# Performance work log

Hardware: AMD Instinct MI355X
Metric: run time of the kernel (lower is better)

## Reference

```python
import jax, jax.numpy as jnp
import numpy as np

N = 50000
E = 800000
F_IN = 500
H = 5          # heads
C = 32         # per-head channels
HID = H * C    # 160
NC = 20        # num_classes
G = 8          # number of graphs in batch
SLOPE_ATT = 0.2   # GATConv attention leaky slope (PyG default)
SLOPE_ACT = 0.01  # F.leaky_relu default


def _layernorm(x, scale, bias, eps=1e-5):
    mu = jnp.mean(x, axis=-1, keepdims=True)
    var = jnp.var(x, axis=-1, keepdims=True)
    return (x - mu) * jax.lax.rsqrt(var + eps) * scale + bias


def _edge_softmax(logits, dst, num_nodes):
    # segment softmax over incoming edges of each destination node
    m = jax.ops.segment_max(logits, dst, num_segments=num_nodes)
    ex = jnp.exp(logits - m[dst])
    s = jax.ops.segment_sum(ex, dst, num_segments=num_nodes)
    return ex / (s[dst] + 1e-16)


def _gat_layer(x, src, dst, W, a_src, a_dst, b):
    n = x.shape[0]
    h = (x @ W).reshape(n, H, C)                       # [N,H,C]
    al_s = jnp.einsum('nhc,hc->nh', h, a_src)          # [N,H]
    al_d = jnp.einsum('nhc,hc->nh', h, a_dst)
    logits = jax.nn.leaky_relu(al_s[src] + al_d[dst], SLOPE_ATT)  # [Et,H]
    alpha = _edge_softmax(logits, dst, n)              # [Et,H]
    msg = h[src] * alpha[..., None]                    # [Et,H,C]
    out = jax.ops.segment_sum(msg, dst, num_segments=n).reshape(n, HID) + b
    return out, alpha


def setup_inputs():
    key = jax.random.key(0)
    ks = jax.random.split(key, 24)
    p = lambda k, shp: jax.random.normal(k, shp, jnp.float32) * 0.05
    x = jax.random.normal(ks[0], (N, F_IN), jnp.float32)
    edge_index = jax.random.randint(ks[1], (2, E), 0, N, jnp.int64)
    batch = jnp.sort(jax.random.randint(ks[2], (N,), 0, G, jnp.int64))
    return {
        'x': x, 'edge_index': edge_index, 'batch': batch,
        'W1': p(ks[3], (F_IN, HID)), 'a_src1': p(ks[4], (H, C)), 'a_dst1': p(ks[5], (H, C)), 'b1': jnp.zeros((HID,), jnp.float32),
        'ln1_s': jnp.ones((HID,), jnp.float32), 'ln1_b': jnp.zeros((HID,), jnp.float32),
        'W2': p(ks[6], (HID, HID)), 'a_src2': p(ks[7], (H, C)), 'a_dst2': p(ks[8], (H, C)), 'b2': jnp.zeros((HID,), jnp.float32),
        'ln2_s': jnp.ones((HID,), jnp.float32), 'ln2_b': jnp.zeros((HID,), jnp.float32),
        'Wm': p(ks[9], (HID, HID)), 'bm': jnp.zeros((HID,), jnp.float32),
        'Wmlp1': p(ks[10], (HID, HID)), 'bmlp1': jnp.zeros((HID,), jnp.float32),
        'ln3_s': jnp.ones((HID,), jnp.float32), 'ln3_b': jnp.zeros((HID,), jnp.float32),
        'Wmlp2': p(ks[11], (HID, NC)), 'bmlp2': jnp.zeros((NC,), jnp.float32),
    }


def reference(x, edge_index, batch, W1, a_src1, a_dst1, b1, ln1_s, ln1_b,
              W2, a_src2, a_dst2, b2, ln2_s, ln2_b, Wm, bm,
              Wmlp1, bmlp1, ln3_s, ln3_b, Wmlp2, bmlp2):
    n = x.shape[0]
    # PyG GATConv adds self-loops by default
    loops = jnp.arange(n, dtype=edge_index.dtype)
    src = jnp.concatenate([edge_index[0], loops])
    dst = jnp.concatenate([edge_index[1], loops])

    h1, alpha1 = _gat_layer(x, src, dst, W1, a_src1, a_dst1, b1)
    h1 = jax.nn.leaky_relu(h1, SLOPE_ACT)
    h1 = _layernorm(h1, ln1_s, ln1_b)      # dropout = identity at eval

    h2, alpha2 = _gat_layer(h1, src, dst, W2, a_src2, a_dst2, b2)
    h2 = jax.nn.leaky_relu(h2, SLOPE_ACT)
    h2 = _layernorm(h2, ln2_s, ln2_b)

    xo = jax.nn.leaky_relu(h2 @ Wm + bm, SLOPE_ACT)   # [N,HID]

    # global_mean_pool over batch assignment
    sums = jax.ops.segment_sum(xo, batch, num_segments=G)
    cnts = jax.ops.segment_sum(jnp.ones((n, 1), xo.dtype), batch, num_segments=G)
    pooled = sums / jnp.maximum(cnts, 1.0)            # [G,HID]

    z = pooled @ Wmlp1 + bmlp1
    z = jax.nn.relu(_layernorm(z, ln3_s, ln3_b))
    rec = z @ Wmlp2 + bmlp2                           # [G,NC]
    return xo, rec, alpha1, alpha2
```

## Files before the change

### kernel.cpp

```cpp
#include <hip/hip_runtime.h>
#include <hip/hip_bf16.h>
#include <cstdint>
#include <cstddef>

#define NN   50000
#define EE   800000
#define ET_  (EE + NN)
#define FIN  500
#define HID_ 160
#define NC_  20
#define GG   8
#define GB1  ((NN + 63) / 64)
#define NK1  16
#define NK2  5

typedef __attribute__((ext_vector_type(8))) short ab8;
typedef __attribute__((ext_vector_type(4))) float f4;

static __device__ __forceinline__ unsigned short f2bf(float v) {
    union { float f; uint32_t u; } c; c.f = v;
    uint32_t r = c.u + 0x7FFFu + ((c.u >> 16) & 1u);
    return (unsigned short)(r >> 16);
}

static __device__ __forceinline__ float2 bf2f2(uint32_t u) {
    union { uint32_t u; float f; } a, b;
    a.u = u << 16;
    b.u = u & 0xffff0000u;
    return make_float2(a.f, b.f);
}

static __device__ __forceinline__ int lbound_i(const int* arr, int n, int val) {
    int lo = 0, hi = n;
    while (lo < hi) { int mid = (lo + hi) >> 1; if (arr[mid] < val) lo = mid + 1; else hi = mid; }
    return lo;
}

__global__ __launch_bounds__(256) void k_hist(const int* __restrict__ ei, int* __restrict__ deg) {
    int e = blockIdx.x * 256 + threadIdx.x;
    if (e >= ET_) return;
    int d = (e < EE) ? ei[EE + e] : (e - EE);
    atomicAdd(&deg[d], 1);
}

__global__ __launch_bounds__(256) void k_scan1(const int* __restrict__ deg, int* __restrict__ rowptr,
                                               int* __restrict__ bsum) {
    __shared__ int s[256];
    int t = threadIdx.x;
    int base = blockIdx.x * 1024 + t * 4;
    int v0 = (base + 0 < NN) ? deg[base + 0] : 0;
    int v1 = (base + 1 < NN) ? deg[base + 1] : 0;
    int v2 = (base + 2 < NN) ? deg[base + 2] : 0;
    int v3 = (base + 3 < NN) ? deg[base + 3] : 0;
    int tot = v0 + v1 + v2 + v3;
    s[t] = tot;
    __syncthreads();
    for (int off = 1; off < 256; off <<= 1) {
        int y = (t >= off) ? s[t - off] : 0;
        __syncthreads();
        s[t] += y;
        __syncthreads();
    }
    int excl = s[t] - tot;
    if (t == 255) bsum[blockIdx.x] = s[255];
    if (base + 0 < NN) rowptr[base + 0] = excl;  excl += v0;
    if (base + 1 < NN) rowptr[base + 1] = excl;  excl += v1;
    if (base + 2 < NN) rowptr[base + 2] = excl;  excl += v2;
    if (base + 3 < NN) rowptr[base + 3] = excl;
}

__global__ void k_scan2(int* __restrict__ bsum, int nb) {
    int t = threadIdx.x;
    int v = (t < nb) ? bsum[t] : 0;
    int orig = v;
    for (int off = 1; off < 64; off <<= 1) {
        int y = __shfl_up(v, off);
        if (t >= off) v += y;
    }
    if (t < nb) bsum[t] = v - orig;
}

__global__ __launch_bounds__(256) void k_scan3(int* __restrict__ rowptr, const int* __restrict__ bsum,
                                               int* __restrict__ cursor) {
    int i = blockIdx.x * 256 + threadIdx.x;
    if (i < NN) {
        int r = rowptr[i] + bsum[i >> 10];
        rowptr[i] = r;
        cursor[i] = r;
    }
    if (i == NN) rowptr[NN] = ET_;
}

__global__ __launch_bounds__(256) void k_scatter(const int* __restrict__ ei, int* __restrict__ cursor,
                                                 int* __restrict__ esrc) {
    int e = blockIdx.x * 256 + threadIdx.x;
    if (e >= ET_) return;
    int s, d;
    if (e < EE) { s = ei[e]; d = ei[EE + e]; } else { s = e - EE; d = e - EE; }
    int slot = atomicAdd(&cursor[d], 1);
    esrc[slot] = s;
}

__global__ __launch_bounds__(256) void k_prep_all(const float* __restrict__ W1, ab8* __restrict__ B1,
                                                  const float* __restrict__ W2, ab8* __restrict__ B2,
                                                  const float* __restrict__ Wm, ab8* __restrict__ Bm,
                                                  float* __restrict__ pooled) {
    int idx = blockIdx.x * 256 + threadIdx.x;
    if (idx < GG * HID_) pooled[idx] = 0.f;
    const int C1 = NK1 * 10 * 64;
    const int C2 = NK2 * 10 * 64;
    const float* W; ab8* Bo; int K, cidx;
    if (idx < C1)                { W = W1; Bo = B1; K = FIN;  cidx = idx; }
    else if (idx < C1 + C2)      { W = W2; Bo = B2; K = HID_; cidx = idx - C1; }
    else if (idx < C1 + 2 * C2)  { W = Wm; Bo = Bm; K = HID_; cidx = idx - C1 - C2; }
    else return;
    int s = cidx / 640, r = cidx % 640;
    int t = r >> 6, l = r & 63;
    int fr = l & 15, q = l >> 4;
    int n  = t * 16 + fr;
    int k0 = s * 32 + q * 8;
    unsigned short pk[8];
#pragma unroll
    for (int j = 0; j < 8; j++) {
        int k = k0 + j;
        pk[j] = (k < K) ? f2bf(W[(size_t)k * HID_ + n]) : (unsigned short)0;
    }
    Bo[cidx] = *reinterpret_cast<ab8*>(pk);
}

__global__ __launch_bounds__(256) void k_conv_x(const float* __restrict__ x, ab8* __restrict__ Apk) {
    int idx = blockIdx.x * 256 + threadIdx.x;
    int tid = idx & 255;
    int s   = (idx >> 8) & (NK1 - 1);
    int blk = idx >> 12;
    int l = tid & 63, w = tid >> 6;
    int fr = l & 15, q = l >> 4;
    int row = blk * 64 + w * 16 + fr;
    int k0 = s * 32 + q * 8;
    unsigned short pk[8] = {0, 0, 0, 0, 0, 0, 0, 0};
    if (row < NN) {
        const float* xr = &x[(size_t)row * FIN];
        if (k0 + 8 <= FIN) {
            const float4* s4 = reinterpret_cast<const float4*>(&xr[k0]);
            float4 u = s4[0], v = s4[1];
            pk[0] = f2bf(u.x); pk[1] = f2bf(u.y); pk[2] = f2bf(u.z); pk[3] = f2bf(u.w);
            pk[4] = f2bf(v.x); pk[5] = f2bf(v.y); pk[6] = f2bf(v.z); pk[7] = f2bf(v.w);
        } else {
#pragma unroll
            for (int j = 0; j < 8; j++)
                if (k0 + j < FIN) pk[j] = f2bf(xr[k0 + j]);
        }
    }
    Apk[idx] = *reinterpret_cast<ab8*>(pk);
}

static __device__ __forceinline__ void gemm_body(const ab8* __restrict__ Apk,
                                                 const ab8* __restrict__ Bpk, int nk,
                                                 float* __restrict__ C, __hip_bfloat16* __restrict__ Cb,
                                                 int M,
                                                 const float* __restrict__ bias, int act,
                                                 const float* __restrict__ asrc, const float* __restrict__ adst,
                                                 float* __restrict__ als_o, float* __restrict__ ald_o,
                                                 const int* __restrict__ batch_p, float* __restrict__ pooled) {
    int tid  = threadIdx.x;
    int lane = tid & 63;
    int w    = tid >> 6;
    int fr   = lane & 15;
    int q    = lane >> 4;
    int row0 = blockIdx.x * 64;

    f4 acc[10];
#pragma unroll
    for (int t = 0; t < 10; t++) acc[t] = (f4)0.f;

    const ab8* bb  = Bpk + lane;
    const ab8* apk = Apk + (size_t)blockIdx.x * nk * 256 + tid;

    ab8 bcur[10], bnx[10];
#pragma unroll
    for (int t = 0; t < 10; t++) bcur[t] = bb[t * 64];
    ab8 a0 = apk[0];
    ab8 a1 = apk[256];
    for (int s = 0; s < nk; s++) {
        if (s + 1 < nk) {
#pragma unroll
            for (int t = 0; t < 10; t++) bnx[t] = bb[((s + 1) * 10 + t) * 64];
        }
        ab8 a2 = (ab8)0;
        if (s + 2 < nk) a2 = apk[(s + 2) * 256];
#pragma unroll
        for (int t = 0; t < 10; t++)
            acc[t] = __builtin_amdgcn_mfma_f32_16x16x32_bf16(a0, bcur[t], acc[t], 0, 0, 0);
        a0 = a1; a1 = a2;
#pragma unroll
        for (int t = 0; t < 10; t++) bcur[t] = bnx[t];
    }

    if (als_o) {
        float av_s[10], av_d[10];
#pragma unroll
        for (int t = 0; t < 10; t++) { av_s[t] = asrc[t * 16 + fr]; av_d[t] = adst[t * 16 + fr]; }
#pragma unroll
        for (int i = 0; i < 4; i++) {
            int r = row0 + w * 16 + q * 4 + i;
            float ps[5], pd[5];
#pragma unroll
            for (int h = 0; h < 5; h++) {
                ps[h] = acc[2 * h][i] * av_s[2 * h] + acc[2 * h + 1][i] * av_s[2 * h + 1];
                pd[h] = acc[2 * h][i] * av_d[2 * h] + acc[2 * h + 1][i] * av_d[2 * h + 1];
            }
#pragma unroll
            for (int off = 8; off >= 1; off >>= 1)
#pragma unroll
                for (int h = 0; h < 5; h++) {
                    ps[h] += __shfl_xor(ps[h], off);
                    pd[h] += __shfl_xor(pd[h], off);
                }
            if (fr == 0 && r < M) {
#pragma unroll
                for (int h = 0; h < 5; h++) {
                    als_o[(size_t)r * 8 + h] = ps[h];
                    ald_o[(size_t)r * 8 + h] = pd[h];
                }
            }
        }
    }

    int gu = -2;
    if (pooled) {
        int rhi = row0 + 63; if (rhi >= M) rhi = M - 1;
        int gl = batch_p[row0], gh = batch_p[rhi];
        gu = (gl == gh) ? gl : -1;
    }
    float psum[10];
#pragma unroll
    for (int t = 0; t < 10; t++) psum[t] = 0.f;

    int rbase = row0 + w * 16 + q * 4;
#pragma unroll
    for (int t = 0; t < 10; t++) {
        int col = t * 16 + fr;
        float bv = bias ? bias[col] : 0.f;
#pragma unroll
        for (int i = 0; i < 4; i++) {
            int r = rbase + i;
            float v = acc[t][i] + bv;
            if (act) v = v > 0.f ? v : 0.01f * v;
            if (r < M) {
                if (C)  C[(size_t)r * HID_ + col] = v;
                if (Cb) *reinterpret_cast<unsigned short*>(&Cb[(size_t)r * HID_ + col]) = f2bf(v);
                if (gu >= 0) psum[t] += v;
                else if (gu == -1) atomicAdd(&pooled[batch_p[r] * HID_ + col], v);
            }
        }
    }
    if (gu >= 0) {
#pragma unroll
        for (int t = 0; t < 10; t++) {
            psum[t] += __shfl_xor(psum[t], 16);
            psum[t] += __shfl_xor(psum[t], 32);
        }
        if (q == 0) {
#pragma unroll
            for (int t = 0; t < 10; t++)
                atomicAdd(&pooled[gu * HID_ + t * 16 + fr], psum[t]);
        }
    }
}

__global__ __launch_bounds__(256) void k_gemm_pk(const ab8* __restrict__ Apk,
                                                 const ab8* __restrict__ Bpk, int nk,
                                                 float* __restrict__ C, __hip_bfloat16* __restrict__ Cb,
                                                 int M,
                                                 const float* __restrict__ bias, int act,
                                                 const float* __restrict__ asrc, const float* __restrict__ adst,
                                                 float* __restrict__ als_o, float* __restrict__ ald_o,
                                                 const int* __restrict__ batch_p, float* __restrict__ pooled) {
    gemm_body(Apk, Bpk, nk, C, Cb, M, bias, act, asrc, adst, als_o, ald_o, batch_p, pooled);
}

__global__ __launch_bounds__(256) void k_att_agg(const int* __restrict__ rowptr,
                                                 const int* __restrict__ esrc,
                                                 const float* __restrict__ als, const float* __restrict__ ald,
                                                 const __hip_bfloat16* __restrict__ hmat,
                                                 float* __restrict__ alphap,
                                                 float* __restrict__ invb,
                                                 const float* __restrict__ bias,
                                                 const float* __restrict__ lns, const float* __restrict__ lnb,
                                                 uint4* __restrict__ xpk) {
    __shared__ float sExp[4][64 * 5];
    __shared__ int   sSrc[4][64];
    int wv   = threadIdx.x >> 6;
    int lane = threadIdx.x & 63;
    int node = blockIdx.x * 4 + wv;
    if (node >= NN) return;
    int start = rowptr[node], end = rowptr[node + 1];
    int deg = end - start;
    bool fits = (deg <= 64);
    float4 dd4 = *reinterpret_cast<const float4*>(&ald[(size_t)node * 8]);
    float  dd5 = ald[(size_t)node * 8 + 4];
    float ad[5] = {dd4.x, dd4.y, dd4.z, dd4.w, dd5};

    float sm[5] = {0.f, 0.f, 0.f, 0.f, 0.f};
    for (int j = start + lane; j < end; j += 64) {
        int sy = esrc[j];
        int idx = j - start;
        if (fits) sSrc[wv][idx] = sy;
        const float* as = &als[(size_t)sy * 8];
        float4 a4 = *reinterpret_cast<const float4*>(as);
        float  a5 = as[4];
        float asv[5] = {a4.x, a4.y, a4.z, a4.w, a5};
#pragma unroll
        for (int h = 0; h < 5; h++) {
            float l = asv[h] + ad[h];
            l = l > 0.f ? l : 0.2f * l;
            float ex = __expf(fminf(l, 60.f));
            sm[h] += ex;
            if (fits) sExp[wv][idx * 5 + h] = ex;
            else      alphap[(size_t)j * 5 + h] = ex;
        }
    }
#pragma unroll
    for (int off = 32; off >= 1; off >>= 1)
#pragma unroll
        for (int h = 0; h < 5; h++) sm[h] += __shfl_xor(sm[h], off);
    float inv[5];
#pragma unroll
    for (int h = 0; h < 5; h++) inv[h] = 1.f / (sm[h] + 1e-16f);
    if (lane == 0) {
        float* ip = &invb[(size_t)node * 8];
        ip[0] = inv[0]; ip[1] = inv[1]; ip[2] = inv[2]; ip[3] = inv[3]; ip[4] = inv[4];
    }
    if (fits && lane < deg) {
#pragma unroll
        for (int h = 0; h < 5; h++) sExp[wv][lane * 5 + h] *= inv[h];
    }

    int h0 = lane >> 4;
    bool lo16 = lane < 16;
    int c01 = 2 * lane;
    int c2  = 128 + 2 * lane;
    float2 A0 = make_float2(0.f, 0.f), A1 = make_float2(0.f, 0.f);
    float2 A2 = make_float2(0.f, 0.f), A3 = make_float2(0.f, 0.f);
    float2 H0 = make_float2(0.f, 0.f), H1 = make_float2(0.f, 0.f);
    float2 H2 = make_float2(0.f, 0.f), H3 = make_float2(0.f, 0.f);

    if (fits) {
        int idx = 0;
        for (; idx + 3 < deg; idx += 4) {
            int s0 = sSrc[wv][idx], s1 = sSrc[wv][idx + 1];
            int s2 = sSrc[wv][idx + 2], s3 = sSrc[wv][idx + 3];
            float w0 = sExp[wv][(idx + 0) * 5 + h0];
            float w1 = sExp[wv][(idx + 1) * 5 + h0];
            float w2 = sExp[wv][(idx + 2) * 5 + h0];
            float w3 = sExp[wv][(idx + 3) * 5 + h0];
            const unsigned short* r0 = (const unsigned short*)&hmat[(size_t)s0 * HID_];
            const unsigned short* r1 = (const unsigned short*)&hmat[(size_t)s1 * HID_];
            const unsigned short* r2 = (const unsigned short*)&hmat[(size_t)s2 * HID_];
            const unsigned short* r3 = (const unsigned short*)&hmat[(size_t)s3 * HID_];
            float2 f0 = bf2f2(*reinterpret_cast<const uint32_t*>(&r0[c01]));
            float2 f1 = bf2f2(*reinterpret_cast<const uint32_t*>(&r1[c01]));
            float2 f2 = bf2f2(*reinterpret_cast<const uint32_t*>(&r2[c01]));
            float2 f3 = bf2f2(*reinterpret_cast<const uint32_t*>(&r3[c01]));
            A0.x += w0 * f0.x; A0.y += w0 * f0.y;
            A1.x += w1 * f1.x; A1.y += w1 * f1.y;
            A2.x += w2 * f2.x; A2.y += w2 * f2.y;
            A3.x += w3 * f3.x; A3.y += w3 * f3.y;
            if (lo16) {
                float u0 = sExp[wv][(idx + 0) * 5 + 4];
                float u1 = sExp[wv][(idx + 1) * 5 + 4];
                float u2 = sExp[wv][(idx + 2) * 5 + 4];
                float u3 = sExp[wv][(idx + 3) * 5 + 4];
                float2 g0 = bf2f2(*reinterpret_cast<const uint32_t*>(&r0[c2]));
                float2 g1 = bf2f2(*reinterpret_cast<const uint32_t*>(&r1[c2]));
                float2 g2 = bf2f2(*reinterpret_cast<const uint32_t*>(&r2[c2]));
                float2 g3 = bf2f2(*reinterpret_cast<const uint32_t*>(&r3[c2]));
                H0.x += u0 * g0.x; H0.y += u0 * g0.y;
                H1.x += u1 * g1.x; H1.y += u1 * g1.y;
                H2.x += u2 * g2.x; H2.y += u2 * g2.y;
                H3.x += u3 * g3.x; H3.y += u3 * g3.y;
            }
        }
        for (; idx < deg; idx++) {
            int s0 = sSrc[wv][idx];
            float w0 = sExp[wv][idx * 5 + h0];
            const unsigned short* r0 = (const unsigned short*)&hmat[(size_t)s0 * HID_];
            float2 f0 = bf2f2(*reinterpret_cast<const uint32_t*>(&r0[c01]));
            A0.x += w0 * f0.x; A0.y += w0 * f0.y;
            if (lo16) {
                float u0 = sExp[wv][idx * 5 + 4];
                float2 g0 = bf2f2(*reinterpret_cast<const uint32_t*>(&r0[c2]));
                H0.x += u0 * g0.x; H0.y += u0 * g0.y;
            }
        }
    } else {
        for (int j = start; j < end; j++) {
            int s0 = esrc[j];
            float w0 = alphap[(size_t)j * 5 + h0] * inv[h0];
            const unsigned short* r0 = (const unsigned short*)&hmat[(size_t)s0 * HID_];
            float2 f0 = bf2f2(*reinterpret_cast<const uint32_t*>(&r0[c01]));
            A0.x += w0 * f0.x; A0.y += w0 * f0.y;
            if (lo16) {
                float u0 = alphap[(size_t)j * 5 + 4] * inv[4];
                float2 g0 = bf2f2(*reinterpret_cast<const uint32_t*>(&r0[c2]));
                H0.x += u0 * g0.x; H0.y += u0 * g0.y;
            }
        }
    }
    float2 A = make_float2(A0.x + A1.x + A2.x + A3.x, A0.y + A1.y + A2.y + A3.y);
    float2 Hh = make_float2(H0.x + H1.x + H2.x + H3.x, H0.y + H1.y + H2.y + H3.y);

    float2 bb = *reinterpret_cast<const float2*>(&bias[c01]);
    float v0 = A.x + bb.x;  v0 = v0 > 0.f ? v0 : 0.01f * v0;
    float v1 = A.y + bb.y;  v1 = v1 > 0.f ? v1 : 0.01f * v1;
    float v2 = 0.f, v3 = 0.f;
    if (lo16) {
        float2 b2 = *reinterpret_cast<const float2*>(&bias[c2]);
        v2 = Hh.x + b2.x; v2 = v2 > 0.f ? v2 : 0.01f * v2;
        v3 = Hh.y + b2.y; v3 = v3 > 0.f ? v3 : 0.01f * v3;
    }
    float s  = v0 + v1 + v2 + v3;
    float sq = v0 * v0 + v1 * v1 + v2 * v2 + v3 * v3;
#pragma unroll
    for (int off = 32; off >= 1; off >>= 1) {
        s  += __shfl_xor(s, off);
        sq += __shfl_xor(sq, off);
    }
    float m = s * (1.f / 160.f);
    float r = rsqrtf(sq * (1.f / 160.f) - m * m + 1e-5f);
    uint32_t pk1, pk2 = 0u;
    {
        float2 sc = *reinterpret_cast<const float2*>(&lns[c01]);
        float2 bi = *reinterpret_cast<const float2*>(&lnb[c01]);
        pk1 = (uint32_t)f2bf((v0 - m) * r * sc.x + bi.x)
            | ((uint32_t)f2bf((v1 - m) * r * sc.y + bi.y) << 16);
    }
    if (lo16) {
        float2 sc = *reinterpret_cast<const float2*>(&lns[c2]);
        float2 bi = *reinterpret_cast<const float2*>(&lnb[c2]);
        pk2 = (uint32_t)f2bf((v2 - m) * r * sc.x + bi.x)
            | ((uint32_t)f2bf((v3 - m) * r * sc.y + bi.y) << 16);
    }
    int j = lane;
    int srcb = (j < 16) ? (4 * j) : (4 * ((j - 16) & 15));
    uint32_t a0w = __shfl(pk1, srcb + 0), a1w = __shfl(pk1, srcb + 1);
    uint32_t a2w = __shfl(pk1, srcb + 2), a3w = __shfl(pk1, srcb + 3);
    uint32_t b0w = __shfl(pk2, srcb + 0), b1w = __shfl(pk2, srcb + 1);
    uint32_t b2w = __shfl(pk2, srcb + 2), b3w = __shfl(pk2, srcb + 3);
    if (j < 20) {
        uint4 val;
        val.x = (j < 16) ? a0w : b0w;
        val.y = (j < 16) ? a1w : b1w;
        val.z = (j < 16) ? a2w : b2w;
        val.w = (j < 16) ? a3w : b3w;
        int blk = node >> 6, wq = (node >> 4) & 3, fr = node & 15;
        int ks = j >> 2, q = j & 3;
        size_t cidx = (size_t)(blk * NK2 + ks) * 256 + wq * 64 + q * 16 + fr;
        xpk[cidx] = val;
    }
}

__global__ __launch_bounds__(256) void k_alpha(const int* __restrict__ ei,
                                               const float* __restrict__ als, const float* __restrict__ ald,
                                               const float* __restrict__ invb,
                                               float* __restrict__ alpha_out) {
    int e = blockIdx.x * 256 + threadIdx.x;
    if (e >= ET_) return;
    int s, d;
    if (e < EE) { s = ei[e]; d = ei[EE + e]; } else { s = e - EE; d = e - EE; }
    const float* as = &als[(size_t)s * 8];
    float4 a4 = *reinterpret_cast<const float4*>(as);
    float  a5 = as[4];
    float asv[5] = {a4.x, a4.y, a4.z, a4.w, a5};
    const float* adp = &ald[(size_t)d * 8];
    float4 d4 = *reinterpret_cast<const float4*>(adp);
    float  d5 = adp[4];
    float adv[5] = {d4.x, d4.y, d4.z, d4.w, d5};
    const float* ip = &invb[(size_t)d * 8];
    float4 i4 = *reinterpret_cast<const float4*>(ip);
    float  i5 = ip[4];
    float ivv[5] = {i4.x, i4.y, i4.z, i4.w, i5};
    float* ao = &alpha_out[(size_t)e * 5];
#pragma unroll
    for (int h = 0; h < 5; h++) {
        float l = asv[h] + adv[h];
        l = l > 0.f ? l : 0.2f * l;
        float ex = __expf(fminf(l, 60.f));
        ao[h] = ex * ivv[h];
    }
}

__global__ __launch_bounds__(256) void k_mlp(const float* __restrict__ pooled, const int* __restrict__ batch,
                                             const float* __restrict__ W1, const float* __restrict__ b1,
                                             const float* __restrict__ lns, const float* __restrict__ lnb,
                                             const float* __restrict__ W2, const float* __restrict__ b2,
                                             float* __restrict__ rec) {
    __shared__ float P[GG][HID_];
    __shared__ float Z[GG][HID_];
    __shared__ float mu[GG], rr[GG], ic[GG];
    int t = threadIdx.x;
    if (t < GG) {
        int lo = lbound_i(batch, NN, t), hi = lbound_i(batch, NN, t + 1);
        ic[t] = 1.f / fmaxf((float)(hi - lo), 1.f);
    }
    __syncthreads();
    for (int i = t; i < GG * HID_; i += 256) P[i / HID_][i % HID_] = pooled[i] * ic[i / HID_];
    __syncthreads();
    for (int i = t; i < GG * HID_; i += 256) {
        int g = i / HID_, j = i % HID_;
        float acc = b1[j];
        for (int k = 0; k < HID_; k++) acc += P[g][k] * W1[k * HID_ + j];
        Z[g][j] = acc;
    }
    __syncthreads();
    if (t < GG) {
        float s = 0.f, sq = 0.f;
        for (int k = 0; k < HID_; k++) { float z = Z[t][k]; s += z; sq += z * z; }
        float m = s / (float)HID_;
        mu[t] = m;
        rr[t] = rsqrtf(sq / (float)HID_ - m * m + 1e-5f);
    }
    __syncthreads();
    for (int i = t; i < GG * HID_; i += 256) {
        int g = i / HID_, j = i % HID_;
        float z = (Z[g][j] - mu[g]) * rr[g] * lns[j] + lnb[j];
        Z[g][j] = fmaxf(z, 0.f);
    }
    __syncthreads();
    for (int i = t; i < GG * NC_; i += 256) {
        int g = i / NC_, j = i % NC_;
        float acc = b2[j];
        for (int k = 0; k < HID_; k++) acc += Z[g][k] * W2[k * NC_ + j];
        rec[g * NC_ + j] = acc;
    }
}

extern "C" void kernel_launch(void* const* d_in, const int* in_sizes, int n_in,
                              void* d_out, int out_size, void* d_ws, size_t ws_size,
                              hipStream_t stream) {
    const float* x    = (const float*)d_in[0];
    const int*   ei   = (const int*)d_in[1];
    const int*   batch= (const int*)d_in[2];
    const float* W1   = (const float*)d_in[3];
    const float* as1  = (const float*)d_in[4];
    const float* ad1  = (const float*)d_in[5];
    const float* b1   = (const float*)d_in[6];
    const float* ln1s = (const float*)d_in[7];
    const float* ln1b = (const float*)d_in[8];
    const float* W2   = (const float*)d_in[9];
    const float* as2  = (const float*)d_in[10];
    const float* ad2  = (const float*)d_in[11];
    const float* b2   = (const float*)d_in[12];
    const float* ln2s = (const float*)d_in[13];
    const float* ln2b = (const float*)d_in[14];
    const float* Wm   = (const float*)d_in[15];
    const float* bm   = (const float*)d_in[16];
    const float* Wm1  = (const float*)d_in[17];
    const float* bm1  = (const float*)d_in[18];
    const float* ln3s = (const float*)d_in[19];
    const float* ln3b = (const float*)d_in[20];
    const float* Wm2  = (const float*)d_in[21];
    const float* bm2  = (const float*)d_in[22];

    float* out    = (float*)d_out;
    float* xo     = out;
    float* rec    = out + (size_t)NN * HID_;
    float* alpha1 = rec + GG * NC_;
    float* alpha2 = alpha1 + (size_t)ET_ * 5;

    char* w = (char*)d_ws;
    auto carve = [&](size_t bytes) { char* p = w; w += (bytes + 255) & ~(size_t)255; return p; };
    int*   deg    = (int*)carve((size_t)NN * 4);
    int*   rowptr = (int*)carve((size_t)(NN + 1) * 4);
    int*   cursor = (int*)carve((size_t)NN * 4);
    int*   esrc   = (int*)carve((size_t)ET_ * 4);
    int*   bsum   = (int*)carve(64 * 4);
    __hip_bfloat16* hbuf = (__hip_bfloat16*)carve((size_t)NN * HID_ * 2);
    uint4* xpk    = (uint4*)carve((size_t)GB1 * NK2 * 256 * 16);
    float* alphap = (float*)carve((size_t)ET_ * 5 * 4);
    float* als    = (float*)carve((size_t)NN * 8 * 4);
    float* ald    = (float*)carve((size_t)NN * 8 * 4);
    float* invb   = (float*)carve((size_t)NN * 8 * 4);
    float* pooled = (float*)carve((size_t)GG * HID_ * 4);
    ab8*   B1pk   = (ab8*)carve((size_t)NK1 * 10 * 64 * 16);
    ab8*   B2pk   = (ab8*)carve((size_t)NK2 * 10 * 64 * 16);
    ab8*   Bmpk   = (ab8*)carve((size_t)NK2 * 10 * 64 * 16);
    ab8*   Apk    = (ab8*)d_out;

    hipMemsetAsync(deg, 0, (size_t)NN * 4, stream);
    k_hist<<<(ET_ + 255) / 256, 256, 0, stream>>>(ei, deg);
    int nb = (NN + 1023) / 1024;
    k_scan1<<<nb, 256, 0, stream>>>(deg, rowptr, bsum);
    k_scan2<<<1, 64, 0, stream>>>(bsum, nb);
    k_scan3<<<(NN + 1 + 255) / 256, 256, 0, stream>>>(rowptr, bsum, cursor);
    k_scatter<<<(ET_ + 255) / 256, 256, 0, stream>>>(ei, cursor, esrc);

    const int PREP = NK1 * 10 * 64 + 2 * NK2 * 10 * 64;
    k_prep_all<<<(PREP + 255) / 256, 256, 0, stream>>>(W1, B1pk, W2, B2pk, Wm, Bmpk, pooled);
    k_conv_x<<<GB1 * NK1, 256, 0, stream>>>(x, Apk);

    const int NWB = (NN + 3) / 4;
    const int EB  = (ET_ + 255) / 256;

    k_gemm_pk<<<GB1, 256, 0, stream>>>(Apk, B1pk, NK1, nullptr, hbuf, NN, nullptr, 0,
                                       as1, ad1, als, ald, nullptr, nullptr);
    k_att_agg<<<NWB, 256, 0, stream>>>(rowptr, esrc, als, ald, hbuf, alphap, invb,
                                       b1, ln1s, ln1b, xpk);
    k_alpha<<<EB, 256, 0, stream>>>(ei, als, ald, invb, alpha1);

    k_gemm_pk<<<GB1, 256, 0, stream>>>((const ab8*)xpk, B2pk, NK2, nullptr, hbuf, NN, nullptr, 0,
                                       as2, ad2, als, ald, nullptr, nullptr);
    k_att_agg<<<NWB, 256, 0, stream>>>(rowptr, esrc, als, ald, hbuf, alphap, invb,
                                       b2, ln2s, ln2b, xpk);
    k_alpha<<<EB, 256, 0, stream>>>(ei, als, ald, invb, alpha2);

    k_gemm_pk<<<GB1, 256, 0, stream>>>((const ab8*)xpk, Bmpk, NK2, xo, nullptr, NN, bm, 1,
                                       nullptr, nullptr, nullptr, nullptr, batch, pooled);
    k_mlp<<<1, 256, 0, stream>>>(pooled, batch, Wm1, bm1, ln3s, ln3b, Wm2, bm2, rec);
}
```

Measured before the change: 643.2 us.

## Horizontally fuse independent kernels to cut launches and overlap small stages

Result: faster. 612.2 us (-4.8%).

```diff
diff --git a/kernel.cpp b/kernel.cpp
--- a/kernel.cpp
+++ b/kernel.cpp
@@ -13,6 +13,7 @@
 #define GB1  ((NN + 63) / 64)
 #define NK1  16
 #define NK2  5
+#define EBH  ((ET_ + 255) / 256)
 
 typedef __attribute__((ext_vector_type(8))) short ab8;
 typedef __attribute__((ext_vector_type(4))) float f4;
@@ -36,11 +37,66 @@
     return lo;
 }
 
-__global__ __launch_bounds__(256) void k_hist(const int* __restrict__ ei, int* __restrict__ deg) {
-    int e = blockIdx.x * 256 + threadIdx.x;
-    if (e >= ET_) return;
-    int d = (e < EE) ? ei[EE + e] : (e - EE);
-    atomicAdd(&deg[d], 1);
+__global__ __launch_bounds__(256) void k_prep0(const float* __restrict__ W1, ab8* __restrict__ B1,
+                                               const float* __restrict__ W2, ab8* __restrict__ B2,
+                                               const float* __restrict__ Wm, ab8* __restrict__ Bm,
+                                               float* __restrict__ pooled, int* __restrict__ deg) {
+    int idx = blockIdx.x * 256 + threadIdx.x;
+    if (idx < NN) deg[idx] = 0;
+    if (idx < GG * HID_) pooled[idx] = 0.f;
+    const int C1 = NK1 * 10 * 64;
+    const int C2 = NK2 * 10 * 64;
+    const float* W; ab8* Bo; int K, cidx;
+    if (idx < C1)                { W = W1; Bo = B1; K = FIN;  cidx = idx; }
+    else if (idx < C1 + C2)      { W = W2; Bo = B2; K = HID_; cidx = idx - C1; }
+    else if (idx < C1 + 2 * C2)  { W = Wm; Bo = Bm; K = HID_; cidx = idx - C1 - C2; }
+    else return;
+    int s = cidx / 640, r = cidx % 640;
+    int t = r >> 6, l = r & 63;
+    int fr = l & 15, q = l >> 4;
+    int n  = t * 16 + fr;
+    int k0 = s * 32 + q * 8;
+    unsigned short pk[8];
+#pragma unroll
+    for (int j = 0; j < 8; j++) {
+        int k = k0 + j;
+        pk[j] = (k < K) ? f2bf(W[(size_t)k * HID_ + n]) : (unsigned short)0;
+    }
+    Bo[cidx] = *reinterpret_cast<ab8*>(pk);
+}
+
+__global__ __launch_bounds__(256) void k_hist_conv(const int* __restrict__ ei, int* __restrict__ deg,
+                                                   const float* __restrict__ x, ab8* __restrict__ Apk) {
+    if (blockIdx.x < EBH) {
+        int e = blockIdx.x * 256 + threadIdx.x;
+        if (e >= ET_) return;
+        int d = (e < EE) ? ei[EE + e] : (e - EE);
+        atomicAdd(&deg[d], 1);
+        return;
+    }
+    int idx = (blockIdx.x - EBH) * 256 + threadIdx.x;
+    int tid = idx & 255;
+    int s   = (idx >> 8) & (NK1 - 1);
+    int blk = idx >> 12;
+    int l = tid & 63, w = tid >> 6;
+    int fr = l & 15, q = l >> 4;
+    int row = blk * 64 + w * 16 + fr;
+    int k0 = s * 32 + q * 8;
+    unsigned short pk[8] = {0, 0, 0, 0, 0, 0, 0, 0};
+    if (row < NN) {
+        const float* xr = &x[(size_t)row * FIN];
+        if (k0 + 8 <= FIN) {
+            const float4* s4 = reinterpret_cast<const float4*>(&xr[k0]);
+            float4 u = s4[0], v = s4[1];
+            pk[0] = f2bf(u.x); pk[1] = f2bf(u.y); pk[2] = f2bf(u.z); pk[3] = f2bf(u.w);
+            pk[4] = f2bf(v.x); pk[5] = f2bf(v.y); pk[6] = f2bf(v.z); pk[7] = f2bf(v.w);
+        } else {
+#pragma unroll
+            for (int j = 0; j < 8; j++)
+                if (k0 + j < FIN) pk[j] = f2bf(xr[k0 + j]);
+        }
+    }
+    Apk[idx] = *reinterpret_cast<ab8*>(pk);
 }
 
 __global__ __launch_bounds__(256) void k_scan1(const int* __restrict__ deg, int* __restrict__ rowptr,
@@ -101,60 +157,8 @@
     esrc[slot] = s;
 }
 
-__global__ __launch_bounds__(256) void k_prep_all(const float* __restrict__ W1, ab8* __restrict__ B1,
-                                                  const float* __restrict__ W2, ab8* __restrict__ B2,
-                                                  const float* __restrict__ Wm, ab8* __restrict__ Bm,
-                                                  float* __restrict__ pooled) {
-    int idx = blockIdx.x * 256 + threadIdx.x;
-    if (idx < GG * HID_) pooled[idx] = 0.f;
-    const int C1 = NK1 * 10 * 64;
-    const int C2 = NK2 * 10 * 64;
-    const float* W; ab8* Bo; int K, cidx;
-    if (idx < C1)                { W = W1; Bo = B1; K = FIN;  cidx = idx; }
-    else if (idx < C1 + C2)      { W = W2; Bo = B2; K = HID_; cidx = idx - C1; }
-    else if (idx < C1 + 2 * C2)  { W = Wm; Bo = Bm; K = HID_; cidx = idx - C1 - C2; }
-    else return;
-    int s = cidx / 640, r = cidx % 640;
-    int t = r >> 6, l = r & 63;
-    int fr = l & 15, q = l >> 4;
-    int n  = t * 16 + fr;
-    int k0 = s * 32 + q * 8;
-    unsigned short pk[8];
-#pragma unroll
-    for (int j = 0; j < 8; j++) {
-        int k = k0 + j;
-        pk[j] = (k < K) ? f2bf(W[(size_t)k * HID_ + n]) : (unsigned short)0;
-    }
-    Bo[cidx] = *reinterpret_cast<ab8*>(pk);
-}
-
-__global__ __launch_bounds__(256) void k_conv_x(const float* __restrict__ x, ab8* __restrict__ Apk) {
-    int idx = blockIdx.x * 256 + threadIdx.x;
-    int tid = idx & 255;
-    int s   = (idx >> 8) & (NK1 - 1);
-    int blk = idx >> 12;
-    int l = tid & 63, w = tid >> 6;
-    int fr = l & 15, q = l >> 4;
-    int row = blk * 64 + w * 16 + fr;
-    int k0 = s * 32 + q * 8;
-    unsigned short pk[8] = {0, 0, 0, 0, 0, 0, 0, 0};
-    if (row < NN) {
-        const float* xr = &x[(size_t)row * FIN];
-        if (k0 + 8 <= FIN) {
-            const float4* s4 = reinterpret_cast<const float4*>(&xr[k0]);
-            float4 u = s4[0], v = s4[1];
-            pk[0] = f2bf(u.x); pk[1] = f2bf(u.y); pk[2] = f2bf(u.z); pk[3] = f2bf(u.w);
-            pk[4] = f2bf(v.x); pk[5] = f2bf(v.y); pk[6] = f2bf(v.z); pk[7] = f2bf(v.w);
-        } else {
-#pragma unroll
-            for (int j = 0; j < 8; j++)
-                if (k0 + j < FIN) pk[j] = f2bf(xr[k0 + j]);
-        }
-    }
-    Apk[idx] = *reinterpret_cast<ab8*>(pk);
-}
-
-static __device__ __forceinline__ void gemm_body(const ab8* __restrict__ Apk,
+static __device__ __forceinline__ void gemm_body(int blk,
+                                                 const ab8* __restrict__ Apk,
                                                  const ab8* __restrict__ Bpk, int nk,
                                                  float* __restrict__ C, __hip_bfloat16* __restrict__ Cb,
                                                  int M,
@@ -167,14 +171,14 @@
     int w    = tid >> 6;
     int fr   = lane & 15;
     int q    = lane >> 4;
-    int row0 = blockIdx.x * 64;
+    int row0 = blk * 64;
 
     f4 acc[10];
 #pragma unroll
     for (int t = 0; t < 10; t++) acc[t] = (f4)0.f;
 
     const ab8* bb  = Bpk + lane;
-    const ab8* apk = Apk + (size_t)blockIdx.x * nk * 256 + tid;
+    const ab8* apk = Apk + (size_t)blk * nk * 256 + tid;
 
     ab8 bcur[10], bnx[10];
 #pragma unroll
@@ -276,7 +280,55 @@
                                                  const float* __restrict__ asrc, const float* __restrict__ adst,
                                                  float* __restrict__ als_o, float* __restrict__ ald_o,
                                                  const int* __restrict__ batch_p, float* __restrict__ pooled) {
-    gemm_body(Apk, Bpk, nk, C, Cb, M, bias, act, asrc, adst, als_o, ald_o, batch_p, pooled);
+    gemm_body(blockIdx.x, Apk, Bpk, nk, C, Cb, M, bias, act, asrc, adst, als_o, ald_o, batch_p, pooled);
+}
+
+static __device__ __forceinline__ void alpha_body(int e, const int* __restrict__ ei,
+                                                  const float* __restrict__ als, const float* __restrict__ ald,
+                                                  const float* __restrict__ invb,
+                                                  float* __restrict__ alpha_out) {
+    if (e >= ET_) return;
+    int s, d;
+    if (e < EE) { s = ei[e]; d = ei[EE + e]; } else { s = e - EE; d = e - EE; }
+    const float* as = &als[(size_t)s * 8];
+    float4 a4 = *reinterpret_cast<const float4*>(as);
+    float  a5 = as[4];
+    float asv[5] = {a4.x, a4.y, a4.z, a4.w, a5};
+    const float* adp = &ald[(size_t)d * 8];
+    float4 d4 = *reinterpret_cast<const float4*>(adp);
+    float  d5 = adp[4];
+    float adv[5] = {d4.x, d4.y, d4.z, d4.w, d5};
+    const float* ip = &invb[(size_t)d * 8];
+    float4 i4 = *reinterpret_cast<const float4*>(ip);
+    float  i5 = ip[4];
+    float ivv[5] = {i4.x, i4.y, i4.z, i4.w, i5};
+    float* ao = &alpha_out[(size_t)e * 5];
+#pragma unroll
+    for (int h = 0; h < 5; h++) {
+        float l = asv[h] + adv[h];
+        l = l > 0.f ? l : 0.2f * l;
+        float ex = __expf(fminf(l, 60.f));
+        ao[h] = ex * ivv[h];
+    }
+}
+
+__global__ __launch_bounds__(256) void k_gemm_alpha(const ab8* __restrict__ Apk,
+                                                    const ab8* __restrict__ Bpk, int nk,
+                                                    float* __restrict__ C, __hip_bfloat16* __restrict__ Cb,
+                                                    int M,
+                                                    const float* __restrict__ bias, int act,
+                                                    const float* __restrict__ asrc, const float* __restrict__ adst,
+                                                    float* __restrict__ als_o, float* __restrict__ ald_o,
+                                                    const int* __restrict__ batch_p, float* __restrict__ pooled,
+                                                    const int* __restrict__ ei,
+                                                    const float* __restrict__ als_r, const float* __restrict__ ald_r,
+                                                    const float* __restrict__ invb, float* __restrict__ alpha_out) {
+    if (blockIdx.x < GB1) {
+        gemm_body(blockIdx.x, Apk, Bpk, nk, C, Cb, M, bias, act, asrc, adst, als_o, ald_o, batch_p, pooled);
+    } else {
+        int e = (blockIdx.x - GB1) * 256 + threadIdx.x;
+        alpha_body(e, ei, als_r, ald_r, invb, alpha_out);
+    }
 }
 
 __global__ __launch_bounds__(256) void k_att_agg(const int* __restrict__ rowptr,
@@ -460,36 +512,6 @@
     }
 }
 
-__global__ __launch_bounds__(256) void k_alpha(const int* __restrict__ ei,
-                                               const float* __restrict__ als, const float* __restrict__ ald,
-                                               const float* __restrict__ invb,
-                                               float* __restrict__ alpha_out) {
-    int e = blockIdx.x * 256 + threadIdx.x;
-    if (e >= ET_) return;
-    int s, d;
-    if (e < EE) { s = ei[e]; d = ei[EE + e]; } else { s = e - EE; d = e - EE; }
-    const float* as = &als[(size_t)s * 8];
-    float4 a4 = *reinterpret_cast<const float4*>(as);
-    float  a5 = as[4];
-    float asv[5] = {a4.x, a4.y, a4.z, a4.w, a5};
-    const float* adp = &ald[(size_t)d * 8];
-    float4 d4 = *reinterpret_cast<const float4*>(adp);
-    float  d5 = adp[4];
-    float adv[5] = {d4.x, d4.y, d4.z, d4.w, d5};
-    const float* ip = &invb[(size_t)d * 8];
-    float4 i4 = *reinterpret_cast<const float4*>(ip);
-    float  i5 = ip[4];
-    float ivv[5] = {i4.x, i4.y, i4.z, i4.w, i5};
-    float* ao = &alpha_out[(size_t)e * 5];
-#pragma unroll
-    for (int h = 0; h < 5; h++) {
-        float l = asv[h] + adv[h];
-        l = l > 0.f ? l : 0.2f * l;
-        float ex = __expf(fminf(l, 60.f));
-        ao[h] = ex * ivv[h];
-    }
-}
-
 __global__ __launch_bounds__(256) void k_mlp(const float* __restrict__ pooled, const int* __restrict__ batch,
                                              const float* __restrict__ W1, const float* __restrict__ b1,
                                              const float* __restrict__ lns, const float* __restrict__ lnb,
@@ -578,8 +600,10 @@
     __hip_bfloat16* hbuf = (__hip_bfloat16*)carve((size_t)NN * HID_ * 2);
     uint4* xpk    = (uint4*)carve((size_t)GB1 * NK2 * 256 * 16);
     float* alphap = (float*)carve((size_t)ET_ * 5 * 4);
-    float* als    = (float*)carve((size_t)NN * 8 * 4);
-    float* ald    = (float*)carve((size_t)NN * 8 * 4);
+    float* als1   = (float*)carve((size_t)NN * 8 * 4);
+    float* ald1   = (float*)carve((size_t)NN * 8 * 4);
+    float* als2   = (float*)carve((size_t)NN * 8 * 4);
+    float* ald2   = (float*)carve((size_t)NN * 8 * 4);
     float* invb   = (float*)carve((size_t)NN * 8 * 4);
     float* pooled = (float*)carve((size_t)GG * HID_ * 4);
     ab8*   B1pk   = (ab8*)carve((size_t)NK1 * 10 * 64 * 16);
@@ -587,34 +611,33 @@
     ab8*   Bmpk   = (ab8*)carve((size_t)NK2 * 10 * 64 * 16);
     ab8*   Apk    = (ab8*)d_out;
 
-    hipMemsetAsync(deg, 0, (size_t)NN * 4, stream);
-    k_hist<<<(ET_ + 255) / 256, 256, 0, stream>>>(ei, deg);
+    k_prep0<<<(NN + 255) / 256, 256, 0, stream>>>(W1, B1pk, W2, B2pk, Wm, Bmpk, pooled, deg);
+
+    k_hist_conv<<<EBH + GB1 * NK1, 256, 0, stream>>>(ei, deg, x, Apk);
+
     int nb = (NN + 1023) / 1024;
     k_scan1<<<nb, 256, 0, stream>>>(deg, rowptr, bsum);
     k_scan2<<<1, 64, 0, stream>>>(bsum, nb);
     k_scan3<<<(NN + 1 + 255) / 256, 256, 0, stream>>>(rowptr, bsum, cursor);
-    k_scatter<<<(ET_ + 255) / 256, 256, 0, stream>>>(ei, cursor, esrc);
-
-    const int PREP = NK1 * 10 * 64 + 2 * NK2 * 10 * 64;
-    k_prep_all<<<(PREP + 255) / 256, 256, 0, stream>>>(W1, B1pk, W2, B2pk, Wm, Bmpk, pooled);
-    k_conv_x<<<GB1 * NK1, 256, 0, stream>>>(x, Apk);
+    k_scatter<<<EBH, 256, 0, stream>>>(ei, cursor, esrc);
 
     const int NWB = (NN + 3) / 4;
-    const int EB  = (ET_ + 255) / 256;
 
     k_gemm_pk<<<GB1, 256, 0, stream>>>(Apk, B1pk, NK1, nullptr, hbuf, NN, nullptr, 0,
-                                       as1, ad1, als, ald, nullptr, nullptr);
-    k_att_agg<<<NWB, 256, 0, stream>>>(rowptr, esrc, als, ald, hbuf, alphap, invb,
+                                       as1, ad1, als1, ald1, nullptr, nullptr);
+    k_att_agg<<<NWB, 256, 0, stream>>>(rowptr, esrc, als1, ald1, hbuf, alphap, invb,
                                        b1, ln1s, ln1b, xpk);
-    k_alpha<<<EB, 256, 0, stream>>>(ei, als, ald, invb, alpha1);
-
-    k_gemm_pk<<<GB1, 256, 0, stream>>>((const ab8*)xpk, B2pk, NK2, nullptr, hbuf, NN, nullptr, 0,
-                                       as2, ad2, als, ald, nullptr, nullptr);
-    k_att_agg<<<NWB, 256, 0, stream>>>(rowptr, esrc, als, ald, hbuf, alphap, invb,
+
+    k_gemm_alpha<<<GB1 + EBH, 256, 0, stream>>>((const ab8*)xpk, B2pk, NK2, nullptr, hbuf, NN,
+                                                nullptr, 0, as2, ad2, als2, ald2, nullptr, nullptr,
+                                                ei, als1, ald1, invb, alpha1);
+
+    k_att_agg<<<NWB, 256, 0, stream>>>(rowptr, esrc, als2, ald2, hbuf, alphap, invb,
                                        b2, ln2s, ln2b, xpk);
-    k_alpha<<<EB, 256, 0, stream>>>(ei, als, ald, invb, alpha2);
-
-    k_gemm_pk<<<GB1, 256, 0, stream>>>((const ab8*)xpk, Bmpk, NK2, xo, nullptr, NN, bm, 1,
-                                       nullptr, nullptr, nullptr, nullptr, batch, pooled);
+
+    k_gemm_alpha<<<GB1 + EBH, 256, 0, stream>>>((const ab8*)xpk, Bmpk, NK2, xo, nullptr, NN,
+                                                bm, 1, nullptr, nullptr, nullptr, nullptr, batch, pooled,
+                                                ei, als2, ald2, invb, alpha2);
+
     k_mlp<<<1, 256, 0, stream>>>(pooled, batch, Wm1, bm1, ln3s, ln3b, Wm2, bm2, rec);
 }
```
